# Kernel optimization log

Hardware: AMD Instinct MI355X
Metric: run time of the kernel (lower is better)

The kernel has to match this reference:

```python
import jax, jax.numpy as jnp
import numpy as np

B, S, D, H = 2, 2048, 1024, 16
HD = D // H
NUM_BUCKETS, MAX_DISTANCE = 32, 128


def setup_inputs() -> dict:
    key = jax.random.key(0)
    ks = jax.random.split(key, 6)
    scale = D ** -0.5
    x = jax.random.normal(ks[0], (B, S, D), dtype=jnp.float32)
    Wq = jax.random.normal(ks[1], (D, D), dtype=jnp.float32) * scale
    Wk = jax.random.normal(ks[2], (D, D), dtype=jnp.float32) * scale
    Wv = jax.random.normal(ks[3], (D, D), dtype=jnp.float32) * scale
    Wo = jax.random.normal(ks[4], (D, D), dtype=jnp.float32) * scale
    rel_emb = jax.random.normal(ks[5], (NUM_BUCKETS, H), dtype=jnp.float32) * 0.02
    # causal mask: True where masked (strictly upper triangular)
    causal_mask = jnp.triu(jnp.ones((S, S), dtype=bool), k=1)
    padding_mask = jnp.zeros((B, S), dtype=bool)  # no PAD tokens
    return {"x": x, "causal_mask": causal_mask, "padding_mask": padding_mask,
            "Wq": Wq, "Wk": Wk, "Wv": Wv, "Wo": Wo, "rel_emb": rel_emb}


def _relative_position_bucket(seq_len: int) -> jnp.ndarray:
    # T5-style bucketing; relative_position = memory - context, n = abs(-rel)
    pos = jnp.arange(seq_len)
    rel = pos[None, :] - pos[:, None]          # (S, S)
    n = jnp.abs(rel)
    max_exact = NUM_BUCKETS // 2
    is_small = n < max_exact
    nf = jnp.maximum(n, 1).astype(jnp.float32)  # avoid log(0); masked by where
    val_if_large = max_exact + (
        jnp.log(nf / max_exact) / np.log(MAX_DISTANCE / max_exact)
        * (NUM_BUCKETS - max_exact)
    ).astype(jnp.int32)
    val_if_large = jnp.minimum(val_if_large, NUM_BUCKETS - 1)
    return jnp.where(is_small, n, val_if_large)


def reference(x, causal_mask, padding_mask, Wq, Wk, Wv, Wo, rel_emb):
    bsz, seq_len, _ = x.shape
    # torch Linear: y = x @ W.T
    q = (x @ Wq.T).reshape(bsz, seq_len, H, HD).transpose(0, 2, 1, 3)
    k = (x @ Wk.T).reshape(bsz, seq_len, H, HD).transpose(0, 2, 1, 3)
    v = (x @ Wv.T).reshape(bsz, seq_len, H, HD).transpose(0, 2, 1, 3)

    scores = jnp.einsum('bhqd,bhkd->bhqk', q, k) / np.sqrt(HD)  # (B,H,S,S)

    buckets = _relative_position_bucket(seq_len)                # (S,S) int
    bias = rel_emb[buckets].transpose(2, 0, 1)[None]            # (1,H,S,S)
    scores = scores + bias

    neg_inf = jnp.array(-jnp.inf, dtype=scores.dtype)
    scores = jnp.where(causal_mask[None, None, :, :], neg_inf, scores)
    scores = jnp.where(padding_mask[:, None, None, :], neg_inf, scores)

    attn = jax.nn.softmax(scores, axis=-1)
    out = jnp.einsum('bhqk,bhkd->bhqd', attn, v)                # (B,H,S,HD)
    out = out.transpose(0, 2, 1, 3).reshape(bsz, seq_len, D)
    return out @ Wo.T
```

## Files before the change

### kernel.cpp

```cpp
#include <hip/hip_runtime.h>
#include <math.h>

#define S_LEN 2048
#define DMODEL 1024
#define NHEAD 16
#define HEADD 64
#define BATCH 2
#define MROWS (BATCH * S_LEN)

typedef __attribute__((ext_vector_type(8))) short bf16x8;
typedef __attribute__((ext_vector_type(4))) float f32x4;
typedef __attribute__((ext_vector_type(4))) unsigned short u16x4;

__device__ __forceinline__ unsigned short f2bf(float f) {
  unsigned int u = __float_as_uint(f);
  u += 0x7fffu + ((u >> 16) & 1u);
  return (unsigned short)(u >> 16);
}

__device__ __forceinline__ unsigned int pk_bf16(float lo, float hi) {
  unsigned int u;
  asm("v_cvt_pk_bf16_f32 %0, %1, %2" : "=v"(u) : "v"(lo), "v"(hi));
  return u;
}

__device__ __forceinline__ void gload_lds16(const void* g, void* l) {
  __builtin_amdgcn_global_load_lds(
      (const __attribute__((address_space(1))) unsigned int*)g,
      (__attribute__((address_space(3))) unsigned int*)l, 16, 0, 0);
}

__global__ void cvt_kernel(const float* __restrict__ src,
                           unsigned short* __restrict__ dst, int n4) {
  int i = blockIdx.x * blockDim.x + threadIdx.x;
  if (i < n4) {
    float4 v = ((const float4*)src)[i];
    u16x4 o;
    o.x = f2bf(v.x); o.y = f2bf(v.y); o.z = f2bf(v.z); o.w = f2bf(v.w);
    ((u16x4*)dst)[i] = o;
  }
}

__global__ void bias_kernel(const float* __restrict__ rel_emb,
                            unsigned short* __restrict__ bias) {
  int i = blockIdx.x * blockDim.x + threadIdx.x;
  if (i >= NHEAD * S_LEN) return;
  int d = i & (S_LEN - 1);
  int h = i >> 11;
  int bucket;
  if (d < 16) {
    bucket = d;
  } else {
    float t = logf((float)d * 0.0625f) / 2.0794415416798357f * 16.0f;
    bucket = 16 + (int)t;
    if (bucket > 31) bucket = 31;
  }
  bias[h * S_LEN + d] = f2bf(rel_emb[bucket * NHEAD + h]);
}

template <typename OT, int MREP>
__global__ __launch_bounds__(256, 3)
void gemm_bt(const unsigned short* __restrict__ A,
             const unsigned short* __restrict__ B0,
             const unsigned short* __restrict__ B1,
             const unsigned short* __restrict__ B2,
             OT* __restrict__ C0, OT* __restrict__ C1, OT* __restrict__ C2,
             int M, int N, int K) {
  constexpr int BM = MREP * 32;
  __shared__ unsigned short As[2][BM * 32];
  __shared__ unsigned short Bs[2][128 * 32];
  const unsigned short* Bt = (blockIdx.z == 0) ? B0 : (blockIdx.z == 1 ? B1 : B2);
  OT* C = (blockIdx.z == 0) ? C0 : (blockIdx.z == 1 ? C1 : C2);
  const int tid = threadIdx.x;
  const int w = tid >> 6, l = tid & 63;
  const int g = l >> 4, c = l & 15;
  const int m0 = blockIdx.y * BM, n0 = blockIdx.x * 128;
  const int wr = (w >> 1) * (BM / 2), wc = (w & 1) * 64;

  f32x4 acc[MREP][4] = {};

  auto stage = [&](int k0, int bu) {
#pragma unroll
    for (int it = 0; it < MREP / 2; ++it) {
      int ti = it * 256 + tid;
      int row = ti >> 2, ch = ti & 3;
      gload_lds16(A + (size_t)(m0 + row) * K + k0 + ch * 8,
                  (char*)As[bu] + (it * 256 + w * 64) * 16);
    }
#pragma unroll
    for (int it = 0; it < 2; ++it) {
      int ti = it * 256 + tid;
      int row = ti >> 2, ch = ti & 3;
      gload_lds16(Bt + (size_t)(n0 + row) * K + k0 + ch * 8,
                  (char*)Bs[bu] + (it * 256 + w * 64) * 16);
    }
  };

  stage(0, 0);
  for (int k0 = 0; k0 < K; k0 += 32) {
    const int bu = (k0 >> 5) & 1;
    asm volatile("s_waitcnt vmcnt(0)" ::: "memory");
    __builtin_amdgcn_sched_barrier(0);
    __builtin_amdgcn_s_barrier();
    if (k0 + 32 < K) stage(k0 + 32, bu ^ 1);

    bf16x8 af[MREP], bfr[4];
#pragma unroll
    for (int mf = 0; mf < MREP; ++mf)
      af[mf] = *(const bf16x8*)((const char*)As[bu] + (wr + mf * 16 + c) * 64 + g * 16);
#pragma unroll
    for (int nf = 0; nf < 4; ++nf)
      bfr[nf] = *(const bf16x8*)((const char*)Bs[bu] + (wc + nf * 16 + c) * 64 + g * 16);
#pragma unroll
    for (int mf = 0; mf < MREP; ++mf)
#pragma unroll
      for (int nf = 0; nf < 4; ++nf)
        acc[mf][nf] = __builtin_amdgcn_mfma_f32_16x16x32_bf16(
            af[mf], bfr[nf], acc[mf][nf], 0, 0, 0);
  }

#pragma unroll
  for (int mf = 0; mf < MREP; ++mf)
#pragma unroll
    for (int nf = 0; nf < 4; ++nf)
#pragma unroll
      for (int r = 0; r < 4; ++r) {
        int row = m0 + wr + mf * 16 + g * 4 + r;
        int col = n0 + wc + nf * 16 + c;
        float v = acc[mf][nf][r];
        if constexpr (sizeof(OT) == 2)
          C[(size_t)row * N + col] = (OT)f2bf(v);
        else
          C[(size_t)row * N + col] = v;
      }
}

__global__ void vtrans_kernel(const unsigned short* __restrict__ V,
                              unsigned short* __restrict__ Vt) {
  __shared__ unsigned short tl[64][72];
  const int tid = threadIdx.x;
  const int bh = blockIdx.y, b = bh >> 4, h = bh & 15;
  const int s0 = blockIdx.x * 64;
  {
    int r = tid >> 2, cq = (tid & 3) * 16;
    const unsigned short* src =
        V + (size_t)(b * S_LEN + s0 + r) * DMODEL + h * HEADD + cq;
    *(bf16x8*)&tl[r][cq] = *(const bf16x8*)src;
    *(bf16x8*)&tl[r][cq + 8] = *(const bf16x8*)(src + 8);
  }
  __syncthreads();
  {
    int hd = tid >> 2, sq = (tid & 3) * 16;
    unsigned short tmp[16];
#pragma unroll
    for (int j = 0; j < 16; ++j) tmp[j] = tl[sq + j][hd];
    unsigned short* dst = Vt + (size_t)(bh * 64 + hd) * S_LEN + s0 + sq;
    *(bf16x8*)dst = *(const bf16x8*)tmp;
    *(bf16x8*)(dst + 8) = *(const bf16x8*)(tmp + 8);
  }
}

__global__ __launch_bounds__(128, 2)
void attn_kernel(const unsigned short* __restrict__ Q,
                 const unsigned short* __restrict__ K,
                 const unsigned short* __restrict__ Vt,
                 const unsigned short* __restrict__ bias,
                 unsigned short* __restrict__ O) {
  __shared__ unsigned short Ks[2][64 * 64];
  __shared__ unsigned short Vs[2][64 * 64];
  __shared__ unsigned short Ps[2][16 * 64];
  __shared__ unsigned short bls[S_LEN];
  const int tid = threadIdx.x;
  const int w = tid >> 6, l = tid & 63;
  const int g = l >> 4, c = l & 15;
  const int bh = blockIdx.y, b = bh >> 4, h = bh & 15;
  const unsigned short* Qb = Q + (size_t)b * S_LEN * DMODEL + h * HEADD;
  const unsigned short* Kb = K + (size_t)b * S_LEN * DMODEL + h * HEADD;
  const unsigned short* Vtb = Vt + (size_t)bh * HEADD * S_LEN;

  {
    const bf16x8* src = (const bf16x8*)(bias + h * S_LEN);
    bf16x8* dst = (bf16x8*)bls;
    dst[tid] = src[tid];
    dst[tid + 128] = src[tid + 128];
  }
  __syncthreads();

  auto stage = [&](int kv0, int bu) {
#pragma unroll
    for (int it = 0; it < 4; ++it) {
      int ti = it * 128 + tid;
      int row = ti >> 3, ch = ti & 7;
      int sch = ch ^ (row & 7);
      gload_lds16(Kb + (size_t)(kv0 + row) * DMODEL + sch * 8,
                  (char*)Ks[bu] + (it * 128 + w * 64) * 16);
      gload_lds16(Vtb + (size_t)row * S_LEN + kv0 + sch * 8,
                  (char*)Vs[bu] + (it * 128 + w * 64) * 16);
    }
  };

  const int pi = blockIdx.x;
#pragma unroll 1
  for (int phase = 0; phase < 2; ++phase) {
    const int qt = phase ? (63 - pi) : pi;
    const int q0 = qt * 32;
    const int nt = qt / 2 + 1;
    const int wrow0 = q0 + w * 16;
    const int qglob = wrow0 + c;

    bf16x8 aq[2];
#pragma unroll
    for (int kh = 0; kh < 2; ++kh)
      aq[kh] = *(const bf16x8*)(Qb + (size_t)qglob * DMODEL + kh * 32 + g * 8);

    f32x4 oacc[4] = {};
    float mreg = -1e30f, lreg = 0.f;

    __builtin_amdgcn_s_barrier();
    stage(0, 0);

#pragma unroll 1
    for (int t = 0; t < nt; ++t) {
      const int kv0 = t * 64;
      const int bu = t & 1;
      asm volatile("s_waitcnt vmcnt(0)" ::: "memory");
      __builtin_amdgcn_sched_barrier(0);
      __builtin_amdgcn_s_barrier();
      if (t + 1 < nt) stage((t + 1) * 64, bu ^ 1);

      f32x4 sac[4] = {};
#pragma unroll
      for (int kh = 0; kh < 2; ++kh) {
        bf16x8 bk[4];
#pragma unroll
        for (int nf = 0; nf < 4; ++nf) {
          int row = nf * 16 + c;
          int off = (row * 128 + (kh * 4 + g) * 16) ^ ((row & 7) << 4);
          bk[nf] = *(const bf16x8*)((const char*)Ks[bu] + off);
        }
#pragma unroll
        for (int nf = 0; nf < 4; ++nf)
          sac[nf] = __builtin_amdgcn_mfma_f32_16x16x32_bf16(
              bk[nf], aq[kh], sac[nf], 0, 0, 0);
      }

      float p[4][4];
      float pmax = -1e30f;
#pragma unroll
      for (int nf = 0; nf < 4; ++nf)
#pragma unroll
        for (int r = 0; r < 4; ++r) {
          int kg = kv0 + nf * 16 + g * 4 + r;
          int d = qglob - kg;
          float bv = __uint_as_float((unsigned int)bls[d < 0 ? 0 : d] << 16);
          float sv = (d >= 0) ? sac[nf][r] * 0.125f + bv : -1e30f;
          p[nf][r] = sv;
          pmax = fmaxf(pmax, sv);
        }
      pmax = fmaxf(pmax, __shfl_xor(pmax, 16));
      pmax = fmaxf(pmax, __shfl_xor(pmax, 32));

      if (!__all(pmax - mreg <= 8.f)) {
        float mnew = fmaxf(mreg, pmax);
        float scl = __expf(mreg - mnew);
        lreg *= scl;
#pragma unroll
        for (int nh = 0; nh < 4; ++nh)
#pragma unroll
          for (int r = 0; r < 4; ++r) oacc[nh][r] *= scl;
        mreg = mnew;
      }
      float lsum = 0.f;
#pragma unroll
      for (int nf = 0; nf < 4; ++nf)
#pragma unroll
        for (int r = 0; r < 4; ++r) {
          float pv = __expf(p[nf][r] - mreg);
          p[nf][r] = pv;
          lsum += pv;
        }
      lsum += __shfl_xor(lsum, 16);
      lsum += __shfl_xor(lsum, 32);
      lreg += lsum;

#pragma unroll
      for (int nf = 0; nf < 4; ++nf) {
        unsigned int u0 = pk_bf16(p[nf][0], p[nf][1]);
        unsigned int u1 = pk_bf16(p[nf][2], p[nf][3]);
        int off = (c * 128 + nf * 32 + g * 8) ^ ((c & 7) << 4);
        *(uint2*)((char*)Ps[w] + off) = make_uint2(u0, u1);
      }

#pragma unroll
      for (int kh = 0; kh < 2; ++kh) {
        bf16x8 pa, va[4];
        {
          int off = (c * 128 + kh * 64 + g * 16) ^ ((c & 7) << 4);
          pa = *(const bf16x8*)((const char*)Ps[w] + off);
        }
#pragma unroll
        for (int nh = 0; nh < 4; ++nh) {
          int row = nh * 16 + c;
          int off = (row * 128 + (kh * 4 + g) * 16) ^ ((row & 7) << 4);
          va[nh] = *(const bf16x8*)((const char*)Vs[bu] + off);
        }
#pragma unroll
        for (int nh = 0; nh < 4; ++nh)
          oacc[nh] = __builtin_amdgcn_mfma_f32_16x16x32_bf16(
              va[nh], pa, oacc[nh], 0, 0, 0);
      }
    }

    {
      float inv = 1.f / lreg;
#pragma unroll
      for (int nh = 0; nh < 4; ++nh) {
        unsigned int u0 = pk_bf16(oacc[nh][0] * inv, oacc[nh][1] * inv);
        unsigned int u1 = pk_bf16(oacc[nh][2] * inv, oacc[nh][3] * inv);
        int off = (c * 128 + nh * 32 + g * 8) ^ ((c & 7) << 4);
        *(uint2*)((char*)Ps[w] + off) = make_uint2(u0, u1);
      }
      int rowq = l >> 2, ch2 = l & 3;
      int off1 = (rowq * 128 + ch2 * 16) ^ ((rowq & 7) << 4);
      int off2 = (rowq * 128 + (ch2 + 4) * 16) ^ ((rowq & 7) << 4);
      bf16x8 o1 = *(const bf16x8*)((const char*)Ps[w] + off1);
      bf16x8 o2 = *(const bf16x8*)((const char*)Ps[w] + off2);
      unsigned short* orow =
          O + (size_t)(b * S_LEN + wrow0 + rowq) * DMODEL + h * HEADD;
      *(bf16x8*)(orow + ch2 * 8) = o1;
      *(bf16x8*)(orow + (ch2 + 4) * 8) = o2;
    }
  }
}

extern "C" void kernel_launch(void* const* d_in, const int* in_sizes, int n_in,
                              void* d_out, int out_size, void* d_ws, size_t ws_size,
                              hipStream_t stream) {
  const float* x   = (const float*)d_in[0];
  const float* Wq  = (const float*)d_in[3];
  const float* Wk  = (const float*)d_in[4];
  const float* Wv  = (const float*)d_in[5];
  const float* Wo  = (const float*)d_in[6];
  const float* rel = (const float*)d_in[7];
  float* out = (float*)d_out;

  char* ws = (char*)d_ws;
  const size_t MB = 1u << 20;
  unsigned short* xb  = (unsigned short*)(ws);
  unsigned short* Oa  = xb;
  unsigned short* Qb  = (unsigned short*)(ws + 8 * MB);
  unsigned short* Kb  = (unsigned short*)(ws + 16 * MB);
  unsigned short* Vb  = (unsigned short*)(ws + 24 * MB);
  unsigned short* Vtb = (unsigned short*)(ws + 32 * MB);
  unsigned short* Wqb = (unsigned short*)(ws + 40 * MB);
  unsigned short* Wkb = (unsigned short*)(ws + 42 * MB);
  unsigned short* Wvb = (unsigned short*)(ws + 44 * MB);
  unsigned short* Wob = (unsigned short*)(ws + 46 * MB);
  unsigned short* bias = (unsigned short*)(ws + 48 * MB);

  cvt_kernel<<<4096, 256, 0, stream>>>(x, xb, 1 << 20);
  cvt_kernel<<<1024, 256, 0, stream>>>(Wq, Wqb, 1 << 18);
  cvt_kernel<<<1024, 256, 0, stream>>>(Wk, Wkb, 1 << 18);
  cvt_kernel<<<1024, 256, 0, stream>>>(Wv, Wvb, 1 << 18);
  cvt_kernel<<<1024, 256, 0, stream>>>(Wo, Wob, 1 << 18);

  bias_kernel<<<128, 256, 0, stream>>>(rel, bias);

  gemm_bt<unsigned short, 4><<<dim3(8, 32, 3), 256, 0, stream>>>(
      xb, Wqb, Wkb, Wvb, Qb, Kb, Vb, MROWS, DMODEL, DMODEL);

  vtrans_kernel<<<dim3(32, 32), 256, 0, stream>>>(Vb, Vtb);

  attn_kernel<<<dim3(32, BATCH * NHEAD), 128, 0, stream>>>(
      Qb, Kb, Vtb, bias, Oa);

  gemm_bt<float, 2><<<dim3(8, 64, 1), 256, 0, stream>>>(
      Oa, Wob, Wob, Wob, out, out, out, MROWS, DMODEL, DMODEL);
}
```

Baseline: 240.6 us.

## Fuse prep kernels, enlarge attention q-tile to 64 rows, fast-path far bias

Merges the five conversion launches and the bias kernel into one prep kernel to cut launch overhead. The attention kernel moves to 256 threads with 64-row query tiles, halving the grid and sharing each staged K/V tile across four waves. Tiles whose relative distances all saturate to bucket 31 skip the masking and bias lookup and use a constant bias. In exchange there are fewer blocks per head and more LDS and registers per block.

Result: faster. 208.5 us (-13.3%).

```diff
diff --git a/kernel.cpp b/kernel.cpp
--- a/kernel.cpp
+++ b/kernel.cpp
@@ -30,32 +30,50 @@
       (__attribute__((address_space(3))) unsigned int*)l, 16, 0, 0);
 }
 
-__global__ void cvt_kernel(const float* __restrict__ src,
-                           unsigned short* __restrict__ dst, int n4) {
-  int i = blockIdx.x * blockDim.x + threadIdx.x;
-  if (i < n4) {
+__global__ void prep_kernel(const float* __restrict__ x,
+                            const float* __restrict__ Wq,
+                            const float* __restrict__ Wk,
+                            const float* __restrict__ Wv,
+                            const float* __restrict__ Wo,
+                            const float* __restrict__ rel,
+                            unsigned short* __restrict__ xb,
+                            unsigned short* __restrict__ Wqb,
+                            unsigned short* __restrict__ Wkb,
+                            unsigned short* __restrict__ Wvb,
+                            unsigned short* __restrict__ Wob,
+                            unsigned short* __restrict__ bias) {
+  int blk = blockIdx.x;
+  if (blk < 8192) {
+    const float* src;
+    unsigned short* dst;
+    int i;
+    if (blk < 4096) {
+      src = x; dst = xb; i = blk * 256 + threadIdx.x;
+    } else {
+      int wsel = (blk - 4096) >> 10;
+      src = (wsel == 0) ? Wq : (wsel == 1) ? Wk : (wsel == 2) ? Wv : Wo;
+      dst = (wsel == 0) ? Wqb : (wsel == 1) ? Wkb : (wsel == 2) ? Wvb : Wob;
+      i = ((blk - 4096) & 1023) * 256 + threadIdx.x;
+    }
     float4 v = ((const float4*)src)[i];
     u16x4 o;
     o.x = f2bf(v.x); o.y = f2bf(v.y); o.z = f2bf(v.z); o.w = f2bf(v.w);
     ((u16x4*)dst)[i] = o;
-  }
-}
-
-__global__ void bias_kernel(const float* __restrict__ rel_emb,
-                            unsigned short* __restrict__ bias) {
-  int i = blockIdx.x * blockDim.x + threadIdx.x;
-  if (i >= NHEAD * S_LEN) return;
-  int d = i & (S_LEN - 1);
-  int h = i >> 11;
-  int bucket;
-  if (d < 16) {
-    bucket = d;
   } else {
-    float t = logf((float)d * 0.0625f) / 2.0794415416798357f * 16.0f;
-    bucket = 16 + (int)t;
-    if (bucket > 31) bucket = 31;
-  }
-  bias[h * S_LEN + d] = f2bf(rel_emb[bucket * NHEAD + h]);
+    int i = (blk - 8192) * 256 + threadIdx.x;
+    if (i >= NHEAD * S_LEN) return;
+    int d = i & (S_LEN - 1);
+    int h = i >> 11;
+    int bucket;
+    if (d < 16) {
+      bucket = d;
+    } else {
+      float t = logf((float)d * 0.0625f) / 2.0794415416798357f * 16.0f;
+      bucket = 16 + (int)t;
+      if (bucket > 31) bucket = 31;
+    }
+    bias[h * S_LEN + d] = f2bf(rel[bucket * NHEAD + h]);
+  }
 }
 
 template <typename OT, int MREP>
@@ -160,7 +178,7 @@
   }
 }
 
-__global__ __launch_bounds__(128, 2)
+__global__ __launch_bounds__(256, 2)
 void attn_kernel(const unsigned short* __restrict__ Q,
                  const unsigned short* __restrict__ K,
                  const unsigned short* __restrict__ Vt,
@@ -168,7 +186,7 @@
                  unsigned short* __restrict__ O) {
   __shared__ unsigned short Ks[2][64 * 64];
   __shared__ unsigned short Vs[2][64 * 64];
-  __shared__ unsigned short Ps[2][16 * 64];
+  __shared__ unsigned short Ps[4][16 * 64];
   __shared__ unsigned short bls[S_LEN];
   const int tid = threadIdx.x;
   const int w = tid >> 6, l = tid & 63;
@@ -178,33 +196,33 @@
   const unsigned short* Kb = K + (size_t)b * S_LEN * DMODEL + h * HEADD;
   const unsigned short* Vtb = Vt + (size_t)bh * HEADD * S_LEN;
 
+  const float bconst =
+      __uint_as_float((unsigned int)bias[h * S_LEN + 1024] << 16);
   {
     const bf16x8* src = (const bf16x8*)(bias + h * S_LEN);
-    bf16x8* dst = (bf16x8*)bls;
-    dst[tid] = src[tid];
-    dst[tid + 128] = src[tid + 128];
+    ((bf16x8*)bls)[tid] = src[tid];
   }
   __syncthreads();
 
   auto stage = [&](int kv0, int bu) {
 #pragma unroll
-    for (int it = 0; it < 4; ++it) {
-      int ti = it * 128 + tid;
+    for (int it = 0; it < 2; ++it) {
+      int ti = it * 256 + tid;
       int row = ti >> 3, ch = ti & 7;
       int sch = ch ^ (row & 7);
       gload_lds16(Kb + (size_t)(kv0 + row) * DMODEL + sch * 8,
-                  (char*)Ks[bu] + (it * 128 + w * 64) * 16);
+                  (char*)Ks[bu] + (it * 256 + w * 64) * 16);
       gload_lds16(Vtb + (size_t)row * S_LEN + kv0 + sch * 8,
-                  (char*)Vs[bu] + (it * 128 + w * 64) * 16);
+                  (char*)Vs[bu] + (it * 256 + w * 64) * 16);
     }
   };
 
   const int pi = blockIdx.x;
 #pragma unroll 1
   for (int phase = 0; phase < 2; ++phase) {
-    const int qt = phase ? (63 - pi) : pi;
-    const int q0 = qt * 32;
-    const int nt = qt / 2 + 1;
+    const int qt = phase ? (31 - pi) : pi;
+    const int q0 = qt * 64;
+    const int nt = qt + 1;
     const int wrow0 = q0 + w * 16;
     const int qglob = wrow0 + c;
 
@@ -246,17 +264,28 @@
 
       float p[4][4];
       float pmax = -1e30f;
-#pragma unroll
-      for (int nf = 0; nf < 4; ++nf)
-#pragma unroll
-        for (int r = 0; r < 4; ++r) {
-          int kg = kv0 + nf * 16 + g * 4 + r;
-          int d = qglob - kg;
-          float bv = __uint_as_float((unsigned int)bls[d < 0 ? 0 : d] << 16);
-          float sv = (d >= 0) ? sac[nf][r] * 0.125f + bv : -1e30f;
-          p[nf][r] = sv;
-          pmax = fmaxf(pmax, sv);
-        }
+      if (kv0 + 176 <= wrow0) {
+#pragma unroll
+        for (int nf = 0; nf < 4; ++nf)
+#pragma unroll
+          for (int r = 0; r < 4; ++r) {
+            float sv = sac[nf][r] * 0.125f + bconst;
+            p[nf][r] = sv;
+            pmax = fmaxf(pmax, sv);
+          }
+      } else {
+#pragma unroll
+        for (int nf = 0; nf < 4; ++nf)
+#pragma unroll
+          for (int r = 0; r < 4; ++r) {
+            int kg = kv0 + nf * 16 + g * 4 + r;
+            int d = qglob - kg;
+            float bv = __uint_as_float((unsigned int)bls[d < 0 ? 0 : d] << 16);
+            float sv = (d >= 0) ? sac[nf][r] * 0.125f + bv : -1e30f;
+            p[nf][r] = sv;
+            pmax = fmaxf(pmax, sv);
+          }
+      }
       pmax = fmaxf(pmax, __shfl_xor(pmax, 16));
       pmax = fmaxf(pmax, __shfl_xor(pmax, 32));
 
@@ -358,20 +387,15 @@
   unsigned short* Wob = (unsigned short*)(ws + 46 * MB);
   unsigned short* bias = (unsigned short*)(ws + 48 * MB);
 
-  cvt_kernel<<<4096, 256, 0, stream>>>(x, xb, 1 << 20);
-  cvt_kernel<<<1024, 256, 0, stream>>>(Wq, Wqb, 1 << 18);
-  cvt_kernel<<<1024, 256, 0, stream>>>(Wk, Wkb, 1 << 18);
-  cvt_kernel<<<1024, 256, 0, stream>>>(Wv, Wvb, 1 << 18);
-  cvt_kernel<<<1024, 256, 0, stream>>>(Wo, Wob, 1 << 18);
-
-  bias_kernel<<<128, 256, 0, stream>>>(rel, bias);
+  prep_kernel<<<8320, 256, 0, stream>>>(x, Wq, Wk, Wv, Wo, rel,
+                                        xb, Wqb, Wkb, Wvb, Wob, bias);
 
   gemm_bt<unsigned short, 4><<<dim3(8, 32, 3), 256, 0, stream>>>(
       xb, Wqb, Wkb, Wvb, Qb, Kb, Vb, MROWS, DMODEL, DMODEL);
 
   vtrans_kernel<<<dim3(32, 32), 256, 0, stream>>>(Vb, Vtb);
 
-  attn_kernel<<<dim3(32, BATCH * NHEAD), 128, 0, stream>>>(
+  attn_kernel<<<dim3(16, BATCH * NHEAD), 256, 0, stream>>>(
       Qb, Kb, Vtb, bias, Oa);
 
   gemm_bt<float, 2><<<dim3(8, 64, 1), 256, 0, stream>>>(
```
